# Performance work log

Measured on AMD Instinct MI355X. Metric: run time of the kernel, lower is better.

The kernel has to match this reference:

```python
import jax, jax.numpy as jnp
import numpy as np

B, C, D, H, W = 2, 128, 16, 16, 16

def setup_inputs() -> dict:
    key = jax.random.key(0)
    ks = jax.random.split(key, 7)
    s = 0.02
    return {
        "x": jax.random.normal(ks[0], (B, C, D, H, W), jnp.float32),
        "Wq": jax.random.normal(ks[1], (C, C), jnp.float32) * s,
        "bq": jax.random.normal(ks[2], (C,), jnp.float32) * s,
        "Wk": jax.random.normal(ks[3], (C, C), jnp.float32) * s,
        "bk": jax.random.normal(ks[4], (C,), jnp.float32) * s,
        "Wv": jax.random.normal(ks[5], (C, C), jnp.float32) * s,
        "bv": jax.random.normal(ks[6], (C,), jnp.float32) * s,
    }

def reference(x, Wq, bq, Wk, bk, Wv, bv):
    b, c, d, h, w = x.shape
    n = d * h * w
    xf = x.reshape(b, c, n)  # [B, C, N]
    # 1x1x1 Conv3d == per-voxel linear over channels
    q = jnp.einsum('oc,bcn->bon', Wq, xf) + bq[None, :, None]
    k = jnp.einsum('oc,bcn->bon', Wk, xf) + bk[None, :, None]
    v = jnp.einsum('oc,bcn->bon', Wv, xf) + bv[None, :, None]
    # energy[b,n,m] = sum_c q[b,c,n] * k[b,c,m]  (no scale, as in source)
    energy = jnp.einsum('bcn,bcm->bnm', q, k)
    attention = jax.nn.softmax(energy, axis=-1)
    # out[b,c,n] = sum_m v[b,c,m] * attention[b,n,m]
    out = jnp.einsum('bcm,bnm->bcn', v, attention)
    return out.reshape(b, c, d, h, w)
```

## Files before the change

kernel.cpp:

```cpp
#include <hip/hip_runtime.h>


typedef __bf16 bf16x8 __attribute__((ext_vector_type(8)));
typedef __bf16 bf16x4v __attribute__((ext_vector_type(4)));
typedef float  f32x4  __attribute__((ext_vector_type(4)));

#define LDP 136
#define LDV 72
#define LDO 33

constexpr int CB = 128;
constexpr int NB = 4096;
constexpr int BB = 2;

__device__ __forceinline__ bf16x8 ldfrag(const __bf16* lds, int row, int koff, int ld) {
  return *(const bf16x8*)(lds + row * ld + koff);
}

__global__ __launch_bounds__(256) void qkv_proj_kernel(
    const float* __restrict__ x,
    const float* __restrict__ Wq, const float* __restrict__ bq,
    const float* __restrict__ Wk, const float* __restrict__ bk,
    const float* __restrict__ Wv, const float* __restrict__ bv,
    __bf16* __restrict__ Qt, __bf16* __restrict__ Kt, __bf16* __restrict__ Vo)
{
  extern __shared__ __align__(16) char smem_raw[];
  __bf16* xT = (__bf16*)smem_raw;
  __bf16* Wl = xT + 64 * LDP;

  const int b  = blockIdx.y;
  const int n0 = blockIdx.x * 64;
  const int m  = blockIdx.z;
  const int t  = threadIdx.x;
  const int lane = t & 63, w = t >> 6;
  const int l15 = lane & 15, quad = lane >> 4;

  const float* W = (m == 0) ? Wq : (m == 1) ? Wk : Wv;
  const float* bias_p = (m == 0) ? bq : (m == 1) ? bk : bv;

  for (int v = t; v < 2048; v += 256) {
    int c = v >> 4, i4 = v & 15;
    float4 d = *(const float4*)(x + (b * CB + c) * NB + n0 + i4 * 4);
    xT[(i4 * 4 + 0) * LDP + c] = (__bf16)d.x;
    xT[(i4 * 4 + 1) * LDP + c] = (__bf16)d.y;
    xT[(i4 * 4 + 2) * LDP + c] = (__bf16)d.z;
    xT[(i4 * 4 + 3) * LDP + c] = (__bf16)d.w;
  }
  for (int v = t; v < 4096; v += 256) {
    int o = v >> 5, c4 = v & 31;
    float4 d = *(const float4*)(W + o * 128 + c4 * 4);
    bf16x4v u = {(__bf16)d.x, (__bf16)d.y, (__bf16)d.z, (__bf16)d.w};
    *(bf16x4v*)(Wl + o * LDP + c4 * 4) = u;
  }
  __syncthreads();

  if (m < 2) {
    f32x4 acc[8];
#pragma unroll
    for (int ct = 0; ct < 8; ct++) acc[ct] = (f32x4)0.0f;
#pragma unroll
    for (int ks = 0; ks < 4; ks++) {
      int koff = ks * 32 + quad * 8;
      bf16x8 a = ldfrag(xT, w * 16 + l15, koff, LDP);
#pragma unroll
      for (int ct = 0; ct < 8; ct++) {
        bf16x8 bb = ldfrag(Wl, ct * 16 + l15, koff, LDP);
        acc[ct] = __builtin_amdgcn_mfma_f32_16x16x32_bf16(a, bb, acc[ct], 0, 0, 0);
      }
    }
    __bf16* O = (m == 0) ? Qt : Kt;
#pragma unroll
    for (int ct = 0; ct < 8; ct++) {
      int o = ct * 16 + l15;
      float bias = bias_p[o];
#pragma unroll
      for (int r = 0; r < 4; r++) {
        int i = w * 16 + quad * 4 + r;
        O[(b * NB + n0 + i) * CB + o] = (__bf16)(acc[ct][r] + bias);
      }
    }
  } else {
    f32x4 acc[2][4];
#pragma unroll
    for (int rr = 0; rr < 2; rr++)
#pragma unroll
      for (int ct = 0; ct < 4; ct++) acc[rr][ct] = (f32x4)0.0f;
#pragma unroll
    for (int ks = 0; ks < 4; ks++) {
      int koff = ks * 32 + quad * 8;
      bf16x8 a0 = ldfrag(Wl, (w * 2 + 0) * 16 + l15, koff, LDP);
      bf16x8 a1 = ldfrag(Wl, (w * 2 + 1) * 16 + l15, koff, LDP);
#pragma unroll
      for (int ct = 0; ct < 4; ct++) {
        bf16x8 bb = ldfrag(xT, ct * 16 + l15, koff, LDP);
        acc[0][ct] = __builtin_amdgcn_mfma_f32_16x16x32_bf16(a0, bb, acc[0][ct], 0, 0, 0);
        acc[1][ct] = __builtin_amdgcn_mfma_f32_16x16x32_bf16(a1, bb, acc[1][ct], 0, 0, 0);
      }
    }
#pragma unroll
    for (int rr = 0; rr < 2; rr++)
#pragma unroll
      for (int ct = 0; ct < 4; ct++)
#pragma unroll
        for (int r = 0; r < 4; r++) {
          int o = (w * 2 + rr) * 16 + quad * 4 + r;
          int i = ct * 16 + l15;
          Vo[(b * CB + o) * NB + n0 + i] = (__bf16)(acc[rr][ct][r] + bias_p[o]);
        }
  }
}

__global__ __launch_bounds__(256, 2) void attn_part_kernel(
    const __bf16* __restrict__ Qt,
    const __bf16* __restrict__ Kt,
    const __bf16* __restrict__ Vo,
    __bf16* __restrict__ Opart, float* __restrict__ Ll, int ksz)
{
  extern __shared__ __align__(16) char smem_raw[];
  __bf16* Kl = (__bf16*)smem_raw;
  __bf16* Vl = Kl + 64 * LDP;
  __bf16* Pl = Vl + 128 * LDV;

  const int b  = blockIdx.y;
  const int q0 = blockIdx.x * 128;
  const int s  = blockIdx.z;
  const int k_base = s * ksz;
  const int nit = ksz >> 6;
  const int t  = threadIdx.x;
  const int lane = t & 63, w = t >> 6;
  const int l15 = lane & 15, quad = lane >> 4;
  const int row0 = w * 32;

  bf16x8 qf[2][4];
#pragma unroll
  for (int st = 0; st < 2; st++)
#pragma unroll
    for (int ks = 0; ks < 4; ks++)
      qf[st][ks] = *(const bf16x8*)(Qt +
          (size_t)(b * NB + q0 + row0 + st * 16 + l15) * CB + ks * 32 + quad * 8);

#pragma unroll
  for (int u = 0; u < 4; u++) {
    int v = t + u * 256;
    int j = v >> 4, c8 = v & 15;
    *(bf16x8*)(Kl + j * LDP + c8 * 8) =
        *(const bf16x8*)(Kt + (size_t)(b * NB + k_base + j) * CB + c8 * 8);
  }
#pragma unroll
  for (int u = 0; u < 4; u++) {
    int v = t + u * 256;
    int c = v >> 3, j8 = v & 7;
    *(bf16x8*)(Vl + c * LDV + j8 * 8) =
        *(const bf16x8*)(Vo + (size_t)(b * CB + c) * NB + k_base + j8 * 8);
  }

  float lsum[2][4] = {{0, 0, 0, 0}, {0, 0, 0, 0}};
  f32x4 o_acc[2][8];
#pragma unroll
  for (int st = 0; st < 2; st++)
#pragma unroll
    for (int tt = 0; tt < 8; tt++) o_acc[st][tt] = (f32x4)0.0f;

  __syncthreads();

  for (int it = 0; it < nit; it++) {
    bf16x8 kr[4], vr[4];
    if (it + 1 < nit) {
      int m1 = k_base + (it + 1) * 64;
#pragma unroll
      for (int u = 0; u < 4; u++) {
        int v = t + u * 256;
        int j = v >> 4, c8 = v & 15;
        kr[u] = *(const bf16x8*)(Kt + (size_t)(b * NB + m1 + j) * CB + c8 * 8);
      }
#pragma unroll
      for (int u = 0; u < 4; u++) {
        int v = t + u * 256;
        int c = v >> 3, j8 = v & 7;
        vr[u] = *(const bf16x8*)(Vo + (size_t)(b * CB + c) * NB + m1 + j8 * 8);
      }
    }

    f32x4 sacc[2][4];
#pragma unroll
    for (int st = 0; st < 2; st++)
#pragma unroll
      for (int tt = 0; tt < 4; tt++) sacc[st][tt] = (f32x4)0.0f;
#pragma unroll
    for (int ks = 0; ks < 4; ks++) {
      int koff = ks * 32 + quad * 8;
#pragma unroll
      for (int tt = 0; tt < 4; tt++) {
        bf16x8 bb = ldfrag(Kl, tt * 16 + l15, koff, LDP);
        sacc[0][tt] = __builtin_amdgcn_mfma_f32_16x16x32_bf16(qf[0][ks], bb, sacc[0][tt], 0, 0, 0);
        sacc[1][tt] = __builtin_amdgcn_mfma_f32_16x16x32_bf16(qf[1][ks], bb, sacc[1][tt], 0, 0, 0);
      }
    }

#pragma unroll
    for (int st = 0; st < 2; st++)
#pragma unroll
      for (int tt = 0; tt < 4; tt++)
#pragma unroll
        for (int r = 0; r < 4; r++) {
          float p = __expf(sacc[st][tt][r]);
          lsum[st][r] += p;
          Pl[(row0 + st * 16 + quad * 4 + r) * LDV + tt * 16 + l15] = (__bf16)p;
        }
    asm volatile("s_waitcnt lgkmcnt(0)" ::: "memory");

#pragma unroll
    for (int ks = 0; ks < 2; ks++) {
      int koff = ks * 32 + quad * 8;
      bf16x8 a0 = ldfrag(Pl, row0 + l15, koff, LDV);
      bf16x8 a1 = ldfrag(Pl, row0 + 16 + l15, koff, LDV);
#pragma unroll
      for (int tt = 0; tt < 8; tt++) {
        bf16x8 bb = ldfrag(Vl, tt * 16 + l15, koff, LDV);
        o_acc[0][tt] = __builtin_amdgcn_mfma_f32_16x16x32_bf16(a0, bb, o_acc[0][tt], 0, 0, 0);
        o_acc[1][tt] = __builtin_amdgcn_mfma_f32_16x16x32_bf16(a1, bb, o_acc[1][tt], 0, 0, 0);
      }
    }

    if (it + 1 < nit) {
      __syncthreads();
#pragma unroll
      for (int u = 0; u < 4; u++) {
        int v = t + u * 256;
        int j = v >> 4, c8 = v & 15;
        *(bf16x8*)(Kl + j * LDP + c8 * 8) = kr[u];
      }
#pragma unroll
      for (int u = 0; u < 4; u++) {
        int v = t + u * 256;
        int c = v >> 3, j8 = v & 7;
        *(bf16x8*)(Vl + c * LDV + j8 * 8) = vr[u];
      }
      __syncthreads();
    }
  }

#pragma unroll
  for (int st = 0; st < 2; st++)
#pragma unroll
    for (int r = 0; r < 4; r++) {
      lsum[st][r] += __shfl_xor(lsum[st][r], 1, 16);
      lsum[st][r] += __shfl_xor(lsum[st][r], 2, 16);
      lsum[st][r] += __shfl_xor(lsum[st][r], 4, 16);
      lsum[st][r] += __shfl_xor(lsum[st][r], 8, 16);
    }

  const size_t obase = ((size_t)(s * BB + b) * NB + q0) * CB;
#pragma unroll
  for (int st = 0; st < 2; st++)
#pragma unroll
    for (int tt = 0; tt < 8; tt++)
#pragma unroll
      for (int r = 0; r < 4; r++)
        Opart[obase + (size_t)(row0 + st * 16 + quad * 4 + r) * CB + tt * 16 + l15] =
            (__bf16)o_acc[st][tt][r];
  if (l15 == 0) {
    const size_t lbase = (size_t)(s * BB + b) * NB + q0 + row0;
#pragma unroll
    for (int st = 0; st < 2; st++)
#pragma unroll
      for (int r = 0; r < 4; r++)
        Ll[lbase + st * 16 + quad * 4 + r] = lsum[st][r];
  }
}

__global__ __launch_bounds__(256) void combine_kernel(
    const __bf16* __restrict__ Opart, const float* __restrict__ Ll,
    float* __restrict__ out, int nsplit)
{
  extern __shared__ __align__(16) char smem_raw[];
  float* Olf = (float*)smem_raw;

  const int b  = blockIdx.y;
  const int n0 = blockIdx.x * 64;
  const int c0 = blockIdx.z * 32;
  const int t  = threadIdx.x;
  const int i  = t >> 2;
  const int cc = (t & 3) * 8;

  float L = 0.0f;
  for (int s = 0; s < nsplit; s++)
    L += Ll[(size_t)(s * BB + b) * NB + n0 + i];

  float acc[8];
#pragma unroll
  for (int u = 0; u < 8; u++) acc[u] = 0.0f;
  for (int s = 0; s < nsplit; s++) {
    bf16x8 d = *(const bf16x8*)(Opart +
        ((size_t)(s * BB + b) * NB + n0 + i) * CB + c0 + cc);
#pragma unroll
    for (int u = 0; u < 8; u++) acc[u] += (float)d[u];
  }
  float invL = 1.0f / L;
#pragma unroll
  for (int u = 0; u < 8; u++) Olf[i * LDO + cc + u] = acc[u] * invL;
  __syncthreads();

  for (int v = t; v < 512; v += 256) {
    int c = v >> 4, i4 = v & 15;
    float4 d;
    d.x = Olf[(i4 * 4 + 0) * LDO + c];
    d.y = Olf[(i4 * 4 + 1) * LDO + c];
    d.z = Olf[(i4 * 4 + 2) * LDO + c];
    d.w = Olf[(i4 * 4 + 3) * LDO + c];
    *(float4*)(out + (size_t)(b * CB + c0 + c) * NB + n0 + i4 * 4) = d;
  }
}

extern "C" void kernel_launch(void* const* d_in, const int* in_sizes, int n_in,
                              void* d_out, int out_size, void* d_ws, size_t ws_size,
                              hipStream_t stream) {
  const float* x  = (const float*)d_in[0];
  const float* Wq = (const float*)d_in[1];
  const float* bq = (const float*)d_in[2];
  const float* Wk = (const float*)d_in[3];
  const float* bk = (const float*)d_in[4];
  const float* Wv = (const float*)d_in[5];
  const float* bv = (const float*)d_in[6];
  float* out = (float*)d_out;

  const size_t qkv_elems = (size_t)BB * NB * CB;
  __bf16* Qt = (__bf16*)d_ws;
  __bf16* Kt = Qt + qkv_elems;
  __bf16* Vo = Kt + qkv_elems;
  char* ws_tail = (char*)(Vo + qkv_elems);
  size_t tail_sz = ws_size - 3 * qkv_elems * sizeof(__bf16);

  const size_t per_split = (size_t)BB * NB * CB * 2 + (size_t)BB * NB * 4;
  int nsplit = 8;
  while (nsplit > 1 && (size_t)nsplit * per_split > tail_sz) nsplit >>= 1;

  __bf16* Opart = (__bf16*)ws_tail;
  float*  Ll = (float*)(Opart + (size_t)nsplit * BB * NB * CB);
  const int ksz = NB / nsplit;

  const int qkv_smem  = (64 * LDP + 128 * LDP) * 2;
  const int attn_smem = (64 * LDP + 128 * LDV + 128 * LDV) * 2;
  const int comb_smem = 64 * LDO * 4;

  qkv_proj_kernel<<<dim3(NB / 64, BB, 3), 256, qkv_smem, stream>>>(
      x, Wq, bq, Wk, bk, Wv, bv, Qt, Kt, Vo);
  attn_part_kernel<<<dim3(NB / 128, BB, nsplit), 256, attn_smem, stream>>>(
      Qt, Kt, Vo, Opart, Ll, ksz);
  combine_kernel<<<dim3(NB / 64, BB, 4), 256, comb_smem, stream>>>(
      Opart, Ll, out, nsplit);
}
```

Measured before the change: 113.9 us.

## Use uneven 12-way key split, drop register prefetch, raise occupancy hint

The attention kernel now splits the 64 key tiles unevenly across gridDim.z splits, and the host asks for 12 splits instead of 8 so the grid better fills the GPU's compute units. The register-staged prefetch of the next K/V tile is removed in favour of a direct load-into-LDS at the top of each iteration. Launch bounds are raised to 3 blocks per SM to cut register pressure and allow more concurrent waves. The trade-off is lost overlap of global loads with MFMA work, which the higher occupancy is meant to hide. It also adds more partial outputs for the combine kernel to read, and the workspace fallback halves 12 to 6 or 3 if memory is short.

```diff
diff --git a/kernel.cpp b/kernel.cpp
--- a/kernel.cpp
+++ b/kernel.cpp
@@ -110,11 +110,11 @@
   }
 }
 
-__global__ __launch_bounds__(256, 2) void attn_part_kernel(
+__global__ __launch_bounds__(256, 3) void attn_part_kernel(
     const __bf16* __restrict__ Qt,
     const __bf16* __restrict__ Kt,
     const __bf16* __restrict__ Vo,
-    __bf16* __restrict__ Opart, float* __restrict__ Ll, int ksz)
+    __bf16* __restrict__ Opart, float* __restrict__ Ll)
 {
   extern __shared__ __align__(16) char smem_raw[];
   __bf16* Kl = (__bf16*)smem_raw;
@@ -124,8 +124,11 @@
   const int b  = blockIdx.y;
   const int q0 = blockIdx.x * 128;
   const int s  = blockIdx.z;
-  const int k_base = s * ksz;
-  const int nit = ksz >> 6;
+  const int nz = gridDim.z;
+  const int per = 64 / nz, rem = 64 % nz;
+  const int tile0 = s * per + (s < rem ? s : rem);
+  const int nit   = per + (s < rem ? 1 : 0);
+  const int k_base = tile0 * 64;
   const int t  = threadIdx.x;
   const int lane = t & 63, w = t >> 6;
   const int l15 = lane & 15, quad = lane >> 4;
@@ -139,21 +142,6 @@
       qf[st][ks] = *(const bf16x8*)(Qt +
           (size_t)(b * NB + q0 + row0 + st * 16 + l15) * CB + ks * 32 + quad * 8);
 
-#pragma unroll
-  for (int u = 0; u < 4; u++) {
-    int v = t + u * 256;
-    int j = v >> 4, c8 = v & 15;
-    *(bf16x8*)(Kl + j * LDP + c8 * 8) =
-        *(const bf16x8*)(Kt + (size_t)(b * NB + k_base + j) * CB + c8 * 8);
-  }
-#pragma unroll
-  for (int u = 0; u < 4; u++) {
-    int v = t + u * 256;
-    int c = v >> 3, j8 = v & 7;
-    *(bf16x8*)(Vl + c * LDV + j8 * 8) =
-        *(const bf16x8*)(Vo + (size_t)(b * CB + c) * NB + k_base + j8 * 8);
-  }
-
   float lsum[2][4] = {{0, 0, 0, 0}, {0, 0, 0, 0}};
   f32x4 o_acc[2][8];
 #pragma unroll
@@ -161,25 +149,24 @@
 #pragma unroll
     for (int tt = 0; tt < 8; tt++) o_acc[st][tt] = (f32x4)0.0f;
 
-  __syncthreads();
-
   for (int it = 0; it < nit; it++) {
-    bf16x8 kr[4], vr[4];
-    if (it + 1 < nit) {
-      int m1 = k_base + (it + 1) * 64;
-#pragma unroll
-      for (int u = 0; u < 4; u++) {
-        int v = t + u * 256;
-        int j = v >> 4, c8 = v & 15;
-        kr[u] = *(const bf16x8*)(Kt + (size_t)(b * NB + m1 + j) * CB + c8 * 8);
-      }
-#pragma unroll
-      for (int u = 0; u < 4; u++) {
-        int v = t + u * 256;
-        int c = v >> 3, j8 = v & 7;
-        vr[u] = *(const bf16x8*)(Vo + (size_t)(b * CB + c) * NB + m1 + j8 * 8);
-      }
-    }
+    const int m0 = k_base + it * 64;
+    if (it > 0) __syncthreads();
+#pragma unroll
+    for (int u = 0; u < 4; u++) {
+      int v = t + u * 256;
+      int j = v >> 4, c8 = v & 15;
+      *(bf16x8*)(Kl + j * LDP + c8 * 8) =
+          *(const bf16x8*)(Kt + (size_t)(b * NB + m0 + j) * CB + c8 * 8);
+    }
+#pragma unroll
+    for (int u = 0; u < 4; u++) {
+      int v = t + u * 256;
+      int c = v >> 3, j8 = v & 7;
+      *(bf16x8*)(Vl + c * LDV + j8 * 8) =
+          *(const bf16x8*)(Vo + (size_t)(b * CB + c) * NB + m0 + j8 * 8);
+    }
+    __syncthreads();
 
     f32x4 sacc[2][4];
 #pragma unroll
@@ -220,23 +207,6 @@
         o_acc[0][tt] = __builtin_amdgcn_mfma_f32_16x16x32_bf16(a0, bb, o_acc[0][tt], 0, 0, 0);
         o_acc[1][tt] = __builtin_amdgcn_mfma_f32_16x16x32_bf16(a1, bb, o_acc[1][tt], 0, 0, 0);
       }
-    }
-
-    if (it + 1 < nit) {
-      __syncthreads();
-#pragma unroll
-      for (int u = 0; u < 4; u++) {
-        int v = t + u * 256;
-        int j = v >> 4, c8 = v & 15;
-        *(bf16x8*)(Kl + j * LDP + c8 * 8) = kr[u];
-      }
-#pragma unroll
-      for (int u = 0; u < 4; u++) {
-        int v = t + u * 256;
-        int c = v >> 3, j8 = v & 7;
-        *(bf16x8*)(Vl + c * LDV + j8 * 8) = vr[u];
-      }
-      __syncthreads();
     }
   }
 
@@ -332,12 +302,11 @@
   size_t tail_sz = ws_size - 3 * qkv_elems * sizeof(__bf16);
 
   const size_t per_split = (size_t)BB * NB * CB * 2 + (size_t)BB * NB * 4;
-  int nsplit = 8;
+  int nsplit = 12;
   while (nsplit > 1 && (size_t)nsplit * per_split > tail_sz) nsplit >>= 1;
 
   __bf16* Opart = (__bf16*)ws_tail;
   float*  Ll = (float*)(Opart + (size_t)nsplit * BB * NB * CB);
-  const int ksz = NB / nsplit;
 
   const int qkv_smem  = (64 * LDP + 128 * LDP) * 2;
   const int attn_smem = (64 * LDP + 128 * LDV + 128 * LDV) * 2;
@@ -346,7 +315,7 @@
   qkv_proj_kernel<<<dim3(NB / 64, BB, 3), 256, qkv_smem, stream>>>(
       x, Wq, bq, Wk, bk, Wv, bv, Qt, Kt, Vo);
   attn_part_kernel<<<dim3(NB / 128, BB, nsplit), 256, attn_smem, stream>>>(
-      Qt, Kt, Vo, Opart, Ll, ksz);
+      Qt, Kt, Vo, Opart, Ll);
   combine_kernel<<<dim3(NB / 64, BB, 4), 256, comb_smem, stream>>>(
       Opart, Ll, out, nsplit);
 }
```

New measurement: 138.6 us. 21.7% more time.
